# Optimization experiments

Measured on AMD Instinct MI355X. Metric: run time of the kernel, lower is better.

## Reference

```python
import jax, jax.numpy as jnp
import numpy as np

N, D = 768, 128  # num_cells, gnn embedding dim (sum(gnn_layers_out_chnls))

def setup_inputs() -> dict:
    key = jax.random.key(0)
    ks = jax.random.split(key, 5)
    z = jax.random.normal(ks[0], (N, D), dtype=jnp.float32)
    W1 = jax.random.normal(ks[1], (256, 2 * D), dtype=jnp.float32) * 0.05
    b1 = jnp.zeros((256,), dtype=jnp.float32)
    W2 = jax.random.normal(ks[2], (128, 256), dtype=jnp.float32) * 0.05
    b2 = jnp.zeros((128,), dtype=jnp.float32)
    Wf = jax.random.normal(ks[3], (2, 128), dtype=jnp.float32) * 0.05
    bf = jnp.zeros((2,), dtype=jnp.float32)
    return {"z": z, "W1": W1, "b1": b1, "W2": W2, "b2": b2, "Wf": Wf, "bf": bf}

def reference(z, W1, b1, W2, b2, Wf, bf):
    # pairs[i, j] = concat(z[j], z[i])  (rtile varies over j, ctile over i)
    # First 1x1 conv over the 2D-channel pair tensor is equivalent to two
    # small matmuls broadcast-summed (same math, avoids N*N*2D materialization).
    d = z.shape[1]
    row_part = jnp.einsum('jd,od->jo', z, W1[:, :d])   # contribution of z[j]
    col_part = jnp.einsum('id,od->io', z, W1[:, d:])   # contribution of z[i]
    h = jax.nn.relu(row_part[None, :, :] + col_part[:, None, :] + b1)  # [N, N, 256]
    # dropout is identity in eval mode (training=False)
    h = jax.nn.relu(jnp.einsum('ijc,oc->ijo', h, W2) + b2)             # [N, N, 128]
    dists = jnp.einsum('ijc,oc->ijo', h, Wf) + bf                      # [N, N, 2]
    return dists
```

## Files before the change

### kernel.cpp

```cpp
#include <hip/hip_runtime.h>


typedef __attribute__((ext_vector_type(8)))  _Float16 f16x8;
typedef __attribute__((ext_vector_type(2)))  float    f32x2;
typedef __attribute__((ext_vector_type(4)))  float    f32x4;

#define NCELL 768
#define DIM   128
#define C1    256
#define C2    128

#define CPL    0
#define TABA   6144
#define TABB   7168
#define CBo    7680
#define LDS_SZ 13824

#define MFMA16(a, b, c) __builtin_amdgcn_mfma_f32_16x16x32_f16(a, b, c, 0, 0, 0)

static __device__ __forceinline__ f32x2 pk_add(f32x2 a, f32x2 b) {
    f32x2 d; asm("v_pk_add_f32 %0, %1, %2" : "=v"(d) : "v"(a), "v"(b)); return d;
}
static __device__ __forceinline__ f32x2 pk_fma(f32x2 a, f32x2 b, f32x2 c) {
    f32x2 d; asm("v_pk_fma_f32 %0, %1, %2, %3" : "=v"(d) : "v"(a), "v"(b), "v"(c)); return d;
}
static __device__ __forceinline__ f32x2 relu2(f32x2 a) {
    f32x2 d; d[0] = fmaxf(a[0], 0.f); d[1] = fmaxf(a[1], 0.f); return d;
}
static __device__ __forceinline__ f32x2 lo2(f32x4 v) { return __builtin_shufflevector(v, v, 0, 1); }
static __device__ __forceinline__ f32x2 hi2(f32x4 v) { return __builtin_shufflevector(v, v, 2, 3); }

__global__ __launch_bounds__(256) void prep_all(const float* __restrict__ z,
                                                const float* __restrict__ W1,
                                                const float* __restrict__ b1,
                                                const float* __restrict__ W2,
                                                _Float16* __restrict__ rp16,
                                                _Float16* __restrict__ cp16,
                                                _Float16* __restrict__ w2h) {
    const int tid = threadIdx.x;
    if (blockIdx.x < 192) {
        const int jb4 = blockIdx.x * 4;
        __shared__ float zl[4 * DIM];
        zl[tid]       = z[(size_t)jb4 * DIM + tid];
        zl[tid + 256] = z[(size_t)jb4 * DIM + tid + 256];
        __syncthreads();
        const int o = tid;
        float a1[4] = {0.f, 0.f, 0.f, 0.f};
        float a2[4] = {0.f, 0.f, 0.f, 0.f};
        const f32x4* w4 = (const f32x4*)(W1 + (size_t)o * (2 * DIM));
#pragma unroll 4
        for (int d4 = 0; d4 < 32; ++d4) {
            f32x4 wa = w4[d4], wb = w4[32 + d4];
#pragma unroll
            for (int jj = 0; jj < 4; ++jj) {
                f32x4 zv = *(const f32x4*)(zl + jj * DIM + d4 * 4);
#pragma unroll
                for (int e = 0; e < 4; ++e) {
                    a1[jj] = fmaf(zv[e], wa[e], a1[jj]);
                    a2[jj] = fmaf(zv[e], wb[e], a2[jj]);
                }
            }
        }
        const float bb = b1[o];
#pragma unroll
        for (int jj = 0; jj < 4; ++jj) {
            rp16[(size_t)(jb4 + jj) * C1 + o] = (_Float16)(a1[jj] + bb);
            cp16[(size_t)(jb4 + jj) * C1 + o] = (_Float16)a2[jj];
        }
    } else {
        const int t = (blockIdx.x - 192) * 256 + tid;
        w2h[t] = (_Float16)W2[t];
    }
}

__global__ __launch_bounds__(256, 3) void pair_head(const _Float16* __restrict__ rp16,
                                                    const _Float16* __restrict__ cp16,
                                                    const _Float16* __restrict__ w2h,
                                                    const float* __restrict__ Wf,
                                                    const float* __restrict__ b2,
                                                    const float* __restrict__ bfv,
                                                    float* __restrict__ out) {
    __shared__ char smem[LDS_SZ];
    const int tid = threadIdx.x;
    const int nh  = tid >> 6;
    const int l   = tid & 63;
    const int lc  = l & 15;
    const int lg  = l >> 4;
    const int jbg = blockIdx.x >> 6;
    const int ic  = blockIdx.x & 63;
    const int j0  = jbg * 16;
    const int i_base = ic * 12;

#pragma unroll
    for (int q = 0; q < 6; ++q) {
        int off = q * 256 + tid;
        ((unsigned*)(smem + CPL))[off] =
            ((const unsigned*)(cp16 + (size_t)i_base * C1))[off];
    }
    if (tid < 64) {
        int n0 = 2 * tid;
        f32x4 A = {b2[n0], b2[n0 + 1], Wf[n0], Wf[n0 + 1]};
        f32x2 B = {Wf[C2 + n0], Wf[C2 + n0 + 1]};
        *(f32x4*)(smem + TABA + tid * 16) = A;
        *(f32x2*)(smem + TABB + tid * 8)  = B;
    }

    f16x8 rpf[8];
#pragma unroll
    for (int ks = 0; ks < 8; ++ks)
        rpf[ks] = *(const f16x8*)(rp16 + (size_t)(j0 + lc) * C1 + lg * 8 + ks * 32);

    f16x8 w2f[2][8];
#pragma unroll
    for (int ng = 0; ng < 2; ++ng)
#pragma unroll
        for (int ks = 0; ks < 8; ++ks)
            w2f[ng][ks] = *(const f16x8*)(w2h + (size_t)(nh * 32 + ng * 16 + lc) * C1 + lg * 8 + ks * 32);

    __syncthreads();

    const f16x8 z8 = (f16x8)(_Float16)0.0f;

#pragma unroll 1
    for (int t = 0; t < 6; ++t) {
        const char* c0 = smem + CPL + (2 * t) * 512 + lg * 16;

        f32x4 ac[2][2];
#pragma unroll
        for (int g = 0; g < 2; ++g)
#pragma unroll
            for (int c = 0; c < 2; ++c) ac[g][c] = (f32x4)0.f;

#pragma unroll
        for (int ks = 0; ks < 8; ++ks) {
            f16x8 cv0 = *(const f16x8*)(c0 + ks * 64);
            f16x8 cv1 = *(const f16x8*)(c0 + 512 + ks * 64);
            f16x8 hb0 = __builtin_elementwise_max(rpf[ks] + cv0, z8);
            ac[0][0] = MFMA16(w2f[0][ks], hb0, ac[0][0]);
            ac[1][0] = MFMA16(w2f[1][ks], hb0, ac[1][0]);
            f16x8 hb1 = __builtin_elementwise_max(rpf[ks] + cv1, z8);
            ac[0][1] = MFMA16(w2f[0][ks], hb1, ac[0][1]);
            ac[1][1] = MFMA16(w2f[1][ks], hb1, ac[1][1]);
        }

        f32x2 P0[2], P1[2];
#pragma unroll
        for (int c = 0; c < 2; ++c) { P0[c] = (f32x2){0.f, 0.f}; P1[c] = (f32x2){0.f, 0.f}; }
#pragma unroll
        for (int ng = 0; ng < 2; ++ng) {
#pragma unroll
            for (int rp2 = 0; rp2 < 2; ++rp2) {
                int np = nh * 16 + ng * 8 + lg * 2 + rp2;
                f32x4 A = *(const f32x4*)(smem + TABA + np * 16);
                f32x2 B = *(const f32x2*)(smem + TABB + np * 8);
#pragma unroll
                for (int c = 0; c < 2; ++c) {
                    f32x2 s = {ac[ng][c][2 * rp2], ac[ng][c][2 * rp2 + 1]};
                    s = relu2(pk_add(s, lo2(A)));
                    P0[c] = pk_fma(hi2(A), s, P0[c]);
                    P1[c] = pk_fma(B, s, P1[c]);
                }
            }
        }
#pragma unroll
        for (int c = 0; c < 2; ++c) {
            float p0 = P0[c][0] + P0[c][1];
            float p1 = P1[c][0] + P1[c][1];
            p0 += __shfl_xor(p0, 16); p1 += __shfl_xor(p1, 16);
            p0 += __shfl_xor(p0, 32); p1 += __shfl_xor(p1, 32);
            if (l < 16) {
                int p = t * 32 + c * 16 + l;
                *(f32x2*)(smem + CBo + nh * 1536 + p * 8) = (f32x2){p0, p1};
            }
        }
    }

    __syncthreads();

    const float bf0 = bfv[0], bf1 = bfv[1];
    if (tid < 192) {
        const int p = tid;
        f32x2 a0 = *(const f32x2*)(smem + CBo +        p * 8);
        f32x2 a1 = *(const f32x2*)(smem + CBo + 1536 + p * 8);
        f32x2 a2 = *(const f32x2*)(smem + CBo + 3072 + p * 8);
        f32x2 a3 = *(const f32x2*)(smem + CBo + 4608 + p * 8);
        float o0 = a0[0] + a1[0] + a2[0] + a3[0] + bf0;
        float o1 = a0[1] + a1[1] + a2[1] + a3[1] + bf1;
        int c = p & 15, ii = (p >> 4) & 1, t = p >> 5;
        int i = i_base + 2 * t + ii;
        int j = j0 + c;
        *(f32x2*)(out + ((size_t)i * NCELL + j) * 2) = (f32x2){o0, o1};
    }
}

extern "C" void kernel_launch(void* const* d_in, const int* in_sizes, int n_in,
                              void* d_out, int out_size, void* d_ws, size_t ws_size,
                              hipStream_t stream) {
    const float* z   = (const float*)d_in[0];
    const float* W1  = (const float*)d_in[1];
    const float* b1  = (const float*)d_in[2];
    const float* W2  = (const float*)d_in[3];
    const float* b2  = (const float*)d_in[4];
    const float* Wf  = (const float*)d_in[5];
    const float* bfv = (const float*)d_in[6];
    float* out = (float*)d_out;

    _Float16* rp16 = (_Float16*)d_ws;
    _Float16* cp16 = rp16 + NCELL * C1;
    _Float16* w2h  = cp16 + NCELL * C1;

    prep_all<<<192 + 128, 256, 0, stream>>>(z, W1, b1, W2, rp16, cp16, w2h);
    pair_head<<<48 * 64, 256, 0, stream>>>(rp16, cp16, w2h, Wf, b2, bfv, out);
}
```

Measured before the change: 66.16 us.

## Software-pipeline MFMA tiles with previous tile's epilogue via double-buffered accumulators

Fully unrolls the six-tile loop and double-buffers the MFMA accumulators so the bias/ReLU/final-projection epilogue and shuffle reduction of tile t-1 are interleaved into the MFMA k-loop of tile t. The goal is to hide VALU and shuffle latency behind matrix-core work instead of serializing them after each tile. The cost is higher register pressure from two accumulator sets plus larger code size, which could hurt occupancy under the 3-waves launch bound.

```diff
diff --git a/kernel.cpp b/kernel.cpp
--- a/kernel.cpp
+++ b/kernel.cpp
@@ -73,6 +73,81 @@
     }
 }
 
+#define JOB(TT, AC, PV, TP, DO_EPI)                                           \
+  {                                                                           \
+    const char* c0 = smem + CPL + (2 * (TT)) * 512 + lg * 16;                 \
+    _Pragma("unroll") for (int g = 0; g < 2; ++g) {                           \
+      AC[g][0] = (f32x4)0.f;                                                  \
+      AC[g][1] = (f32x4)0.f;                                                  \
+    }                                                                         \
+    f32x2 P0[2], P1[2];                                                       \
+    P0[0] = (f32x2){0.f, 0.f}; P0[1] = (f32x2){0.f, 0.f};                     \
+    P1[0] = (f32x2){0.f, 0.f}; P1[1] = (f32x2){0.f, 0.f};                     \
+    _Pragma("unroll") for (int ks = 0; ks < 8; ++ks) {                        \
+      f16x8 cv0 = *(const f16x8*)(c0 + ks * 64);                              \
+      f16x8 cv1 = *(const f16x8*)(c0 + 512 + ks * 64);                        \
+      f16x8 hb0 = __builtin_elementwise_max(rpf[ks] + cv0, z8);               \
+      AC[0][0] = MFMA16(w2f[0][ks], hb0, AC[0][0]);                           \
+      AC[1][0] = MFMA16(w2f[1][ks], hb0, AC[1][0]);                           \
+      f16x8 hb1 = __builtin_elementwise_max(rpf[ks] + cv1, z8);               \
+      AC[0][1] = MFMA16(w2f[0][ks], hb1, AC[0][1]);                           \
+      AC[1][1] = MFMA16(w2f[1][ks], hb1, AC[1][1]);                           \
+      if (DO_EPI) {                                                           \
+        if (ks < 4) {                                                         \
+          const int ng = ks >> 1, rp2 = ks & 1;                               \
+          const int np = nh * 16 + ng * 8 + lg * 2 + rp2;                     \
+          f32x4 A = *(const f32x4*)(smem + TABA + np * 16);                   \
+          f32x2 B = *(const f32x2*)(smem + TABB + np * 8);                    \
+          _Pragma("unroll") for (int c = 0; c < 2; ++c) {                     \
+            f32x2 s = {PV[ng][c][2 * rp2], PV[ng][c][2 * rp2 + 1]};           \
+            s = relu2(pk_add(s, lo2(A)));                                     \
+            P0[c] = pk_fma(hi2(A), s, P0[c]);                                 \
+            P1[c] = pk_fma(B, s, P1[c]);                                      \
+          }                                                                   \
+        } else if (ks == 4 || ks == 5) {                                      \
+          const int c = ks - 4;                                               \
+          float p0 = P0[c][0] + P0[c][1];                                     \
+          float p1 = P1[c][0] + P1[c][1];                                     \
+          p0 += __shfl_xor(p0, 16); p1 += __shfl_xor(p1, 16);                 \
+          p0 += __shfl_xor(p0, 32); p1 += __shfl_xor(p1, 32);                 \
+          if (l < 16) {                                                       \
+            int p = (TP) * 32 + c * 16 + l;                                   \
+            *(f32x2*)(smem + CBo + nh * 1536 + p * 8) = (f32x2){p0, p1};      \
+          }                                                                   \
+        }                                                                     \
+      }                                                                       \
+    }                                                                         \
+  }
+
+#define EPI_TAIL(PV, TP)                                                      \
+  {                                                                           \
+    f32x2 P0[2], P1[2];                                                       \
+    P0[0] = (f32x2){0.f, 0.f}; P0[1] = (f32x2){0.f, 0.f};                     \
+    P1[0] = (f32x2){0.f, 0.f}; P1[1] = (f32x2){0.f, 0.f};                     \
+    _Pragma("unroll") for (int ch = 0; ch < 4; ++ch) {                        \
+      const int ng = ch >> 1, rp2 = ch & 1;                                   \
+      const int np = nh * 16 + ng * 8 + lg * 2 + rp2;                         \
+      f32x4 A = *(const f32x4*)(smem + TABA + np * 16);                       \
+      f32x2 B = *(const f32x2*)(smem + TABB + np * 8);                        \
+      _Pragma("unroll") for (int c = 0; c < 2; ++c) {                         \
+        f32x2 s = {PV[ng][c][2 * rp2], PV[ng][c][2 * rp2 + 1]};               \
+        s = relu2(pk_add(s, lo2(A)));                                         \
+        P0[c] = pk_fma(hi2(A), s, P0[c]);                                     \
+        P1[c] = pk_fma(B, s, P1[c]);                                          \
+      }                                                                       \
+    }                                                                         \
+    _Pragma("unroll") for (int c = 0; c < 2; ++c) {                           \
+      float p0 = P0[c][0] + P0[c][1];                                         \
+      float p1 = P1[c][0] + P1[c][1];                                         \
+      p0 += __shfl_xor(p0, 16); p1 += __shfl_xor(p1, 16);                     \
+      p0 += __shfl_xor(p0, 32); p1 += __shfl_xor(p1, 32);                     \
+      if (l < 16) {                                                           \
+        int p = (TP) * 32 + c * 16 + l;                                       \
+        *(f32x2*)(smem + CBo + nh * 1536 + p * 8) = (f32x2){p0, p1};          \
+      }                                                                       \
+    }                                                                         \
+  }
+
 __global__ __launch_bounds__(256, 3) void pair_head(const _Float16* __restrict__ rp16,
                                                     const _Float16* __restrict__ cp16,
                                                     const _Float16* __restrict__ w2h,
@@ -121,59 +196,15 @@
 
     const f16x8 z8 = (f16x8)(_Float16)0.0f;
 
-#pragma unroll 1
-    for (int t = 0; t < 6; ++t) {
-        const char* c0 = smem + CPL + (2 * t) * 512 + lg * 16;
-
-        f32x4 ac[2][2];
-#pragma unroll
-        for (int g = 0; g < 2; ++g)
-#pragma unroll
-            for (int c = 0; c < 2; ++c) ac[g][c] = (f32x4)0.f;
-
-#pragma unroll
-        for (int ks = 0; ks < 8; ++ks) {
-            f16x8 cv0 = *(const f16x8*)(c0 + ks * 64);
-            f16x8 cv1 = *(const f16x8*)(c0 + 512 + ks * 64);
-            f16x8 hb0 = __builtin_elementwise_max(rpf[ks] + cv0, z8);
-            ac[0][0] = MFMA16(w2f[0][ks], hb0, ac[0][0]);
-            ac[1][0] = MFMA16(w2f[1][ks], hb0, ac[1][0]);
-            f16x8 hb1 = __builtin_elementwise_max(rpf[ks] + cv1, z8);
-            ac[0][1] = MFMA16(w2f[0][ks], hb1, ac[0][1]);
-            ac[1][1] = MFMA16(w2f[1][ks], hb1, ac[1][1]);
-        }
-
-        f32x2 P0[2], P1[2];
-#pragma unroll
-        for (int c = 0; c < 2; ++c) { P0[c] = (f32x2){0.f, 0.f}; P1[c] = (f32x2){0.f, 0.f}; }
-#pragma unroll
-        for (int ng = 0; ng < 2; ++ng) {
-#pragma unroll
-            for (int rp2 = 0; rp2 < 2; ++rp2) {
-                int np = nh * 16 + ng * 8 + lg * 2 + rp2;
-                f32x4 A = *(const f32x4*)(smem + TABA + np * 16);
-                f32x2 B = *(const f32x2*)(smem + TABB + np * 8);
-#pragma unroll
-                for (int c = 0; c < 2; ++c) {
-                    f32x2 s = {ac[ng][c][2 * rp2], ac[ng][c][2 * rp2 + 1]};
-                    s = relu2(pk_add(s, lo2(A)));
-                    P0[c] = pk_fma(hi2(A), s, P0[c]);
-                    P1[c] = pk_fma(B, s, P1[c]);
-                }
-            }
-        }
-#pragma unroll
-        for (int c = 0; c < 2; ++c) {
-            float p0 = P0[c][0] + P0[c][1];
-            float p1 = P1[c][0] + P1[c][1];
-            p0 += __shfl_xor(p0, 16); p1 += __shfl_xor(p1, 16);
-            p0 += __shfl_xor(p0, 32); p1 += __shfl_xor(p1, 32);
-            if (l < 16) {
-                int p = t * 32 + c * 16 + l;
-                *(f32x2*)(smem + CBo + nh * 1536 + p * 8) = (f32x2){p0, p1};
-            }
-        }
-    }
+    f32x4 acA[2][2], acB[2][2];
+
+    JOB(0, acA, acB, 0, 0)
+    JOB(1, acB, acA, 0, 1)
+    JOB(2, acA, acB, 1, 1)
+    JOB(3, acB, acA, 2, 1)
+    JOB(4, acA, acB, 3, 1)
+    JOB(5, acB, acA, 4, 1)
+    EPI_TAIL(acB, 5)
 
     __syncthreads();
 
```

Result: slower. 68.24 us (+3.1%).

## Precompute ReLU hidden tiles cooperatively into double-buffered swizzled LDS

Applied to the files above, without the earlier changes.

Instead of each wave redundantly computing relu(rp+cp) per MFMA operand (four waves repeat the same add/max), the block cooperatively builds the 32-pair hidden tile once into LDS with an XOR swizzle, double-buffered so the next tile's cp loads and h construction overlap current MFMAs. The rp rows move from registers to LDS, freeing VGPRs. This raises LDS use to ~48KB per block, which may cut occupancy below the 3-blocks launch bound, and adds a barrier per iteration.

```diff
diff --git a/kernel.cpp b/kernel.cpp
--- a/kernel.cpp
+++ b/kernel.cpp
@@ -4,17 +4,19 @@
 typedef __attribute__((ext_vector_type(8)))  _Float16 f16x8;
 typedef __attribute__((ext_vector_type(2)))  float    f32x2;
 typedef __attribute__((ext_vector_type(4)))  float    f32x4;
+typedef __attribute__((ext_vector_type(4)))  unsigned u32x4;
 
 #define NCELL 768
 #define DIM   128
 #define C1    256
 #define C2    128
 
-#define CPL    0
-#define TABA   6144
-#define TABB   7168
-#define CBo    7680
-#define LDS_SZ 13824
+#define RPL    0
+#define HT     8192
+#define TABA   40960
+#define TABB   41984
+#define CBo    42496
+#define LDS_SZ 48640
 
 #define MFMA16(a, b, c) __builtin_amdgcn_mfma_f32_16x16x32_f16(a, b, c, 0, 0, 0)
 
@@ -91,11 +93,14 @@
     const int j0  = jbg * 16;
     const int i_base = ic * 12;
 
-#pragma unroll
-    for (int q = 0; q < 6; ++q) {
-        int off = q * 256 + tid;
-        ((unsigned*)(smem + CPL))[off] =
-            ((const unsigned*)(cp16 + (size_t)i_base * C1))[off];
+    const f16x8 z8 = (f16x8)(_Float16)0.0f;
+
+#pragma unroll
+    for (int q = 0; q < 2; ++q) {
+        int ch = q * 256 + tid;
+        int row = ch >> 5, co = (ch & 31) * 16;
+        u32x4 v = *(const u32x4*)((const char*)rp16 + (size_t)(j0 + row) * 512 + co);
+        *(u32x4*)(smem + RPL + row * 512 + co) = v;
     }
     if (tid < 64) {
         int n0 = 2 * tid;
@@ -104,12 +109,6 @@
         *(f32x4*)(smem + TABA + tid * 16) = A;
         *(f32x2*)(smem + TABB + tid * 8)  = B;
     }
-
-    f16x8 rpf[8];
-#pragma unroll
-    for (int ks = 0; ks < 8; ++ks)
-        rpf[ks] = *(const f16x8*)(rp16 + (size_t)(j0 + lc) * C1 + lg * 8 + ks * 32);
-
     f16x8 w2f[2][8];
 #pragma unroll
     for (int ng = 0; ng < 2; ++ng)
@@ -119,11 +118,35 @@
 
     __syncthreads();
 
-    const f16x8 z8 = (f16x8)(_Float16)0.0f;
+#pragma unroll
+    for (int it = 0; it < 4; ++it) {
+        int pr   = (it & 1) * 8 + (tid >> 5);
+        int pair = (it >> 1) * 16 + pr;
+        int co   = (tid & 31) * 16;
+        int i    = i_base + (it >> 1);
+        u32x4 cw = *(const u32x4*)((const char*)cp16 + (size_t)i * 512 + co);
+        f16x8 cv = __builtin_bit_cast(f16x8, cw);
+        f16x8 rv = *(const f16x8*)(smem + RPL + pr * 512 + co);
+        f16x8 h  = __builtin_elementwise_max(rv + cv, z8);
+        *(f16x8*)(smem + HT + pair * 512 + (co ^ ((pair & 7) << 4))) = h;
+    }
+    __syncthreads();
+
+    const float bf0 = bfv[0], bf1 = bfv[1];
 
 #pragma unroll 1
     for (int t = 0; t < 6; ++t) {
-        const char* c0 = smem + CPL + (2 * t) * 512 + lg * 16;
+        u32x4 cpr[4];
+        if (t < 5) {
+#pragma unroll
+            for (int it = 0; it < 4; ++it) {
+                int co = (tid & 31) * 16;
+                int i  = i_base + 2 * (t + 1) + (it >> 1);
+                cpr[it] = *(const u32x4*)((const char*)cp16 + (size_t)i * 512 + co);
+            }
+        }
+
+        const char* hbuf = smem + HT + (t & 1) * 16384;
 
         f32x4 ac[2][2];
 #pragma unroll
@@ -131,14 +154,14 @@
 #pragma unroll
             for (int c = 0; c < 2; ++c) ac[g][c] = (f32x4)0.f;
 
+        const int swz = (lc & 7) << 4;
 #pragma unroll
         for (int ks = 0; ks < 8; ++ks) {
-            f16x8 cv0 = *(const f16x8*)(c0 + ks * 64);
-            f16x8 cv1 = *(const f16x8*)(c0 + 512 + ks * 64);
-            f16x8 hb0 = __builtin_elementwise_max(rpf[ks] + cv0, z8);
+            int off = lg * 16 + ks * 64;
+            f16x8 hb0 = *(const f16x8*)(hbuf + lc * 512 + (off ^ swz));
+            f16x8 hb1 = *(const f16x8*)(hbuf + (16 + lc) * 512 + (off ^ swz));
             ac[0][0] = MFMA16(w2f[0][ks], hb0, ac[0][0]);
             ac[1][0] = MFMA16(w2f[1][ks], hb0, ac[1][0]);
-            f16x8 hb1 = __builtin_elementwise_max(rpf[ks] + cv1, z8);
             ac[0][1] = MFMA16(w2f[0][ks], hb1, ac[0][1]);
             ac[1][1] = MFMA16(w2f[1][ks], hb1, ac[1][1]);
         }
@@ -173,11 +196,24 @@
                 *(f32x2*)(smem + CBo + nh * 1536 + p * 8) = (f32x2){p0, p1};
             }
         }
-    }
-
-    __syncthreads();
-
-    const float bf0 = bfv[0], bf1 = bfv[1];
+
+        if (t < 5) {
+#pragma unroll
+            for (int it = 0; it < 4; ++it) {
+                int pr   = (it & 1) * 8 + (tid >> 5);
+                int pair = (it >> 1) * 16 + pr;
+                int co   = (tid & 31) * 16;
+                f16x8 cv = __builtin_bit_cast(f16x8, cpr[it]);
+                f16x8 rv = *(const f16x8*)(smem + RPL + pr * 512 + co);
+                f16x8 h  = __builtin_elementwise_max(rv + cv, z8);
+                *(f16x8*)(smem + HT + ((t + 1) & 1) * 16384 + pair * 512 +
+                          (co ^ ((pair & 7) << 4))) = h;
+            }
+        }
+
+        __syncthreads();
+    }
+
     if (tid < 192) {
         const int p = tid;
         f32x2 a0 = *(const f32x2*)(smem + CBo +        p * 8);
```

Result: slower. 69.37 us (+4.8%).
